# Kernel tuning notes

Hardware: AMD Instinct MI355X
Metric: run time of the kernel (lower is better)

The kernel has to match this reference:

```python
import jax, jax.numpy as jnp
import numpy as np

HID = 1024  # hidden size of the bilinear interaction space

def setup_inputs() -> dict:
    key = jax.random.key(0)
    k1, k2, kw1, kb1, kw2, kwo, kbo = jax.random.split(key, 7)
    B, N1, N2, D1, D2, OUT = 4, 128, 128, 768, 768, 2
    s1 = 1.0 / np.sqrt(D1)
    s2 = 1.0 / np.sqrt(D2)
    so = 1.0 / np.sqrt(HID)
    return {
        "input1": jax.random.normal(k1, (B, N1, D1), dtype=jnp.float32),
        "input2": jax.random.normal(k2, (B, N2, D2), dtype=jnp.float32),
        # torch nn.Linear convention: weight [out, in], y = x @ W.T + b
        "W1": jax.random.uniform(kw1, (HID, D1), jnp.float32, -s1, s1),
        "b1": jax.random.uniform(kb1, (HID,), jnp.float32, -s1, s1),
        "W2": jax.random.uniform(kw2, (HID, D2), jnp.float32, -s2, s2),  # bias=False
        "Wo": jax.random.uniform(kwo, (OUT, HID), jnp.float32, -so, so),
        "bo": jax.random.uniform(kbo, (OUT,), jnp.float32, -so, so),
    }

def reference(input1, input2, W1, b1, W2, Wo, bo):
    # in1: [B, N1, HID], in2: [B, N2, HID]
    in1 = jnp.einsum("bnd,hd->bnh", input1, W1) + b1
    in2 = jnp.einsum("bmd,hd->bmh", input2, W2)
    # broadcast outer-sum -> [B, N1, N2, HID], ReLU, then project to OUT
    h = jax.nn.relu(in1[:, :, None, :] + in2[:, None, :, :])
    return jnp.einsum("bnmh,oh->bnmo", h, Wo) + bo
```

## Files before the change

kernel.cpp:

```cpp
#include <hip/hip_runtime.h>
#include <hip/hip_bf16.h>


typedef __attribute__((ext_vector_type(8))) short s16x8;
typedef __attribute__((ext_vector_type(4))) float f32x4;

#define KP 2304
#define BK 64
#define KHALF 1152
#define NSTEP (KHALF / BK)

__device__ __forceinline__ void gl_lds16(const void* g, void* l) {
    __builtin_amdgcn_global_load_lds(
        (const __attribute__((address_space(1))) unsigned int*)g,
        (__attribute__((address_space(3))) unsigned int*)l, 16, 0, 0);
}

__global__ __launch_bounds__(256) void prepack(
    const float* __restrict__ in1, const float* __restrict__ in2,
    const float* __restrict__ W1, const float* __restrict__ W2,
    ushort* __restrict__ Abig, ushort* __restrict__ Wbig)
{
    const int gid = blockIdx.x * 256 + threadIdx.x;
    const int src = gid / 196608;
    const int rem = gid % 196608;
    const int row = rem / 192;
    const int k4  = (rem % 192) * 4;
    const float* sp;
    ushort* dst;
    if (src == 0) {
        sp  = (row < 512) ? in1 + (size_t)row * 768 + k4
                          : in2 + (size_t)(row - 512) * 768 + k4;
        dst = Abig + (size_t)row * KP + k4;
    } else {
        sp  = (src == 1 ? W1 : W2) + (size_t)row * 768 + k4;
        dst = Wbig + (size_t)(src - 1) * (1024 * KP) + (size_t)row * KP + k4;
    }
    const float4 x = *(const float4*)sp;
    const float xf[4] = {x.x, x.y, x.z, x.w};
    ushort h[4], l[4];
    #pragma unroll
    for (int i = 0; i < 4; ++i) {
        const float v = xf[i];
        __hip_bfloat16 bh = __float2bfloat16(v);
        const float fh = __bfloat162float(bh);
        __hip_bfloat16 bl = __float2bfloat16(v - fh);
        h[i] = *(ushort*)&bh;
        l[i] = *(ushort*)&bl;
    }
    const ushort4 H = make_ushort4(h[0], h[1], h[2], h[3]);
    const ushort4 L = make_ushort4(l[0], l[1], l[2], l[3]);
    if (src == 0) {
        *(ushort4*)(dst)        = H;
        *(ushort4*)(dst + 768)  = L;
        *(ushort4*)(dst + 1536) = H;
    } else {
        *(ushort4*)(dst)        = H;
        *(ushort4*)(dst + 768)  = H;
        *(ushort4*)(dst + 1536) = L;
    }
}

__global__ __launch_bounds__(512) void gemm_mfma(
    const ushort* __restrict__ Abig, const ushort* __restrict__ Wbig,
    const float* __restrict__ b1, float* __restrict__ hid)
{
    const int t    = threadIdx.x;
    const int lane = t & 63;
    const int w    = t >> 6;
    const int kh   = w >> 2;
    const int ws   = w & 3;
    const int row0 = blockIdx.y * 64;
    const int col0 = blockIdx.x * 64;

    const char* __restrict__ A = (const char*)(Abig + (size_t)row0 * KP);
    const char* __restrict__ W = (const char*)(Wbig
                                   + (row0 < 512 ? (size_t)0 : (size_t)1024 * KP)
                                   + (size_t)col0 * KP);

    __shared__ ushort lds[2][2][2][4096];

    const int srow = t >> 3;
    const int kbyt = (((t & 7) ^ (srow & 7)) << 4);
    const size_t rowoff = (size_t)srow * (KP * 2);

    const int wr = ws >> 1, wc = ws & 1;
    const int l15 = lane & 15, kg = lane >> 4;
    int aoff[2][2], boff[2][2];
    #pragma unroll
    for (int kk = 0; kk < 2; ++kk)
        #pragma unroll
        for (int f = 0; f < 2; ++f) {
            const int r = wr * 32 + f * 16 + l15;
            const int c = wc * 32 + f * 16 + l15;
            const int sw_ = kk * 64 + kg * 16;
            aoff[kk][f] = r * 128 + (sw_ ^ ((r & 7) << 4));
            boff[kk][f] = c * 128 + (sw_ ^ ((c & 7) << 4));
        }

#define STAGE(buf, ktk) do {                                                   \
        const size_t kby = (size_t)(ktk) * (BK * 2);                           \
        _Pragma("unroll")                                                      \
        for (int p = 0; p < 4; ++p) {                                          \
            const char* src = (p & 1) ? W : A;                                 \
            const size_t off = rowoff + (size_t)(p >> 1) * (KHALF * 2)         \
                               + kby + kbyt;                                   \
            gl_lds16(src + off,                                                \
                     (char*)&lds[buf][p >> 1][p & 1][0] + t * 16);             \
        }                                                                      \
    } while (0)

    const f32x4 zero = {0.f, 0.f, 0.f, 0.f};
    f32x4 acc[2][2] = {{zero, zero}, {zero, zero}};

    STAGE(0, 0);
    int cur = 0;
    for (int kt = 0; kt < NSTEP; ++kt) {
        asm volatile("s_waitcnt vmcnt(0)" ::: "memory");
        __syncthreads();
        if (kt + 1 < NSTEP) STAGE(cur ^ 1, kt + 1);
        const char* __restrict__ ab = (const char*)&lds[cur][kh][0][0];
        const char* __restrict__ wb = (const char*)&lds[cur][kh][1][0];
        #pragma unroll
        for (int kk = 0; kk < 2; ++kk) {
            s16x8 af[2], bf_[2];
            #pragma unroll
            for (int f = 0; f < 2; ++f) {
                af[f]  = *(const s16x8*)(ab + aoff[kk][f]);
                bf_[f] = *(const s16x8*)(wb + boff[kk][f]);
            }
            #pragma unroll
            for (int fr = 0; fr < 2; ++fr)
                #pragma unroll
                for (int fc = 0; fc < 2; ++fc)
                    acc[fr][fc] = __builtin_amdgcn_mfma_f32_16x16x32_bf16(
                        af[fr], bf_[fc], acc[fr][fc], 0, 0, 0);
        }
        cur ^= 1;
    }
#undef STAGE

    __syncthreads();
    float* red = (float*)&lds[0][0][0][0];
    if (kh == 1) {
        #pragma unroll
        for (int fr = 0; fr < 2; ++fr)
            #pragma unroll
            for (int fc = 0; fc < 2; ++fc)
                *(f32x4*)&red[(((ws * 2 + fr) * 2 + fc) * 64 + lane) * 4] =
                    acc[fr][fc];
    }
    __syncthreads();
    if (kh == 0) {
        float bias[2] = {0.f, 0.f};
        if (row0 < 512) {
            bias[0] = b1[col0 + wc * 32 + l15];
            bias[1] = b1[col0 + wc * 32 + 16 + l15];
        }
        #pragma unroll
        for (int fr = 0; fr < 2; ++fr)
            #pragma unroll
            for (int fc = 0; fc < 2; ++fc) {
                const f32x4 o = *(const f32x4*)
                    &red[(((ws * 2 + fr) * 2 + fc) * 64 + lane) * 4];
                #pragma unroll
                for (int i = 0; i < 4; ++i) {
                    const int r = row0 + wr * 32 + fr * 16 + kg * 4 + i;
                    const int c = col0 + wc * 32 + fc * 16 + l15;
                    hid[(size_t)r * 1024 + c] = acc[fr][fc][i] + o[i] + bias[fc];
                }
            }
    }
}

__global__ __launch_bounds__(256) void out_init(
    const float* __restrict__ bo, float* __restrict__ out)
{
    const int g = blockIdx.x * 256 + threadIdx.x;
    *(float2*)&out[(size_t)g * 2] = make_float2(bo[0], bo[1]);
}

__global__ __launch_bounds__(256) void pair_kernel(
    const float* __restrict__ hid, const float* __restrict__ Wo,
    float* __restrict__ out)
{
    const int t  = threadIdx.x;
    const int b  = blockIdx.z >> 2;
    const int h0 = (blockIdx.z & 3) * 256;
    const int n0 = blockIdx.y * 16;
    const int m0 = blockIdx.x * 16;

    __shared__ float s1[16][260];
    __shared__ float s2[16][260];
    __shared__ float sw[2][256];

    const float* __restrict__ base1 = hid + ((size_t)(b * 128 + n0)) * 1024 + h0;
    const float* __restrict__ base2 = hid + ((size_t)(512 + b * 128 + m0)) * 1024 + h0;

    #pragma unroll
    for (int p = 0; p < 4; ++p) {
        const int slot = p * 256 + t;
        const int r  = slot >> 6;
        const int c  = (slot & 63) << 2;
        *(float4*)&s1[r][c] = *(const float4*)&base1[(size_t)r * 1024 + c];
        *(float4*)&s2[r][c] = *(const float4*)&base2[(size_t)r * 1024 + c];
    }
    if (t < 128) {
        const int o = t >> 6;
        const int c = (t & 63) << 2;
        *(float4*)&sw[o][c] = *(const float4*)&Wo[(size_t)o * 1024 + h0 + c];
    }
    __syncthreads();

    const int i = t >> 4, j = t & 15;
    const float* __restrict__ xrow = &s1[i][0];
    const float* __restrict__ yrow = &s2[j][0];
    float acc0 = 0.f, acc1 = 0.f;

    #pragma unroll 8
    for (int c4 = 0; c4 < 64; ++c4) {
        const float4 x  = *(const float4*)&xrow[c4 * 4];
        const float4 y  = *(const float4*)&yrow[c4 * 4];
        const float4 uu = *(const float4*)&sw[0][c4 * 4];
        const float4 vv = *(const float4*)&sw[1][c4 * 4];
        float r;
        r = fmaxf(x.x + y.x, 0.f); acc0 = fmaf(r, uu.x, acc0); acc1 = fmaf(r, vv.x, acc1);
        r = fmaxf(x.y + y.y, 0.f); acc0 = fmaf(r, uu.y, acc0); acc1 = fmaf(r, vv.y, acc1);
        r = fmaxf(x.z + y.z, 0.f); acc0 = fmaf(r, uu.z, acc0); acc1 = fmaf(r, vv.z, acc1);
        r = fmaxf(x.w + y.w, 0.f); acc0 = fmaf(r, uu.w, acc0); acc1 = fmaf(r, vv.w, acc1);
    }

    const size_t P = (((size_t)b * 128 + n0 + i) * 128 + (m0 + j)) * 2;
    atomicAdd(&out[P],     acc0);
    atomicAdd(&out[P + 1], acc1);
}

extern "C" void kernel_launch(void* const* d_in, const int* in_sizes, int n_in,
                              void* d_out, int out_size, void* d_ws, size_t ws_size,
                              hipStream_t stream) {
    (void)in_sizes; (void)n_in; (void)out_size; (void)ws_size;
    const float* input1 = (const float*)d_in[0];
    const float* input2 = (const float*)d_in[1];
    const float* W1     = (const float*)d_in[2];
    const float* b1     = (const float*)d_in[3];
    const float* W2     = (const float*)d_in[4];
    const float* Wo     = (const float*)d_in[5];
    const float* bo     = (const float*)d_in[6];
    float* out = (float*)d_out;

    ushort* Abig = (ushort*)d_ws;
    ushort* Wbig = Abig + (size_t)1024 * KP;
    float*  hid  = (float*)(Wbig + (size_t)2 * 1024 * KP);

    prepack<<<2304, 256, 0, stream>>>(input1, input2, W1, W2, Abig, Wbig);
    gemm_mfma<<<dim3(16, 16), 512, 0, stream>>>(Abig, Wbig, b1, hid);
    out_init<<<256, 256, 0, stream>>>(bo, out);
    pair_kernel<<<dim3(8, 8, 16), 256, 0, stream>>>(hid, Wo, out);
}
```

Baseline: 105.9 us.

## Split GEMM K dimension across blocks with atomic accumulation into bias-initialized output

Replaces the in-block two-way K split (512 threads, LDS reduction) with a 6-way split-K across the grid's z dimension, so the GEMM launches 1536 blocks of 256 threads instead of 256 blocks. A new init kernel pre-fills the hidden buffer with the bias (or zero for the second input), and each block atomically adds its partial tile. The double-buffered async prefetch is dropped in favor of a single-buffer load-sync-compute loop. This is meant to fill more compute units, at the cost of an extra kernel launch, float atomics traffic, nondeterministic summation order, and no load/compute overlap inside a block.

```diff
diff --git a/kernel.cpp b/kernel.cpp
--- a/kernel.cpp
+++ b/kernel.cpp
@@ -7,13 +7,25 @@
 
 #define KP 2304
 #define BK 64
-#define KHALF 1152
-#define NSTEP (KHALF / BK)
+#define KSPLIT 6
+#define KRANGE 384
+#define NSTEPK (KRANGE / BK)
 
 __device__ __forceinline__ void gl_lds16(const void* g, void* l) {
     __builtin_amdgcn_global_load_lds(
         (const __attribute__((address_space(1))) unsigned int*)g,
         (__attribute__((address_space(3))) unsigned int*)l, 16, 0, 0);
+}
+
+__global__ __launch_bounds__(256) void hid_init(
+    const float* __restrict__ b1, float* __restrict__ hid)
+{
+    const int g   = blockIdx.x * 256 + threadIdx.x;
+    const int row = g >> 8;
+    const int c4  = (g & 255) << 2;
+    float4 v = make_float4(0.f, 0.f, 0.f, 0.f);
+    if (row < 512) v = *(const float4*)&b1[c4];
+    *(float4*)&hid[(size_t)row * 1024 + c4] = v;
 }
 
 __global__ __launch_bounds__(256) void prepack(
@@ -61,30 +73,33 @@
     }
 }
 
-__global__ __launch_bounds__(512) void gemm_mfma(
+__global__ __launch_bounds__(256) void gemm_mfma(
     const ushort* __restrict__ Abig, const ushort* __restrict__ Wbig,
-    const float* __restrict__ b1, float* __restrict__ hid)
+    float* __restrict__ hid)
 {
     const int t    = threadIdx.x;
     const int lane = t & 63;
     const int w    = t >> 6;
-    const int kh   = w >> 2;
-    const int ws   = w & 3;
     const int row0 = blockIdx.y * 64;
     const int col0 = blockIdx.x * 64;
-
-    const char* __restrict__ A = (const char*)(Abig + (size_t)row0 * KP);
+    const int k0   = blockIdx.z * KRANGE;
+
+    const char* __restrict__ A = (const char*)(Abig + (size_t)row0 * KP + k0);
     const char* __restrict__ W = (const char*)(Wbig
                                    + (row0 < 512 ? (size_t)0 : (size_t)1024 * KP)
-                                   + (size_t)col0 * KP);
-
-    __shared__ ushort lds[2][2][2][4096];
-
-    const int srow = t >> 3;
-    const int kbyt = (((t & 7) ^ (srow & 7)) << 4);
-    const size_t rowoff = (size_t)srow * (KP * 2);
-
-    const int wr = ws >> 1, wc = ws & 1;
+                                   + (size_t)col0 * KP + k0);
+
+    __shared__ ushort lds[2][4096];
+
+    int srow[2], cbyt[2];
+    #pragma unroll
+    for (int q = 0; q < 2; ++q) {
+        const int slot = q * 256 + t;
+        srow[q] = slot >> 3;
+        cbyt[q] = ((slot & 7) ^ (srow[q] & 7)) << 4;
+    }
+
+    const int wr = w >> 1, wc = w & 1;
     const int l15 = lane & 15, kg = lane >> 4;
     int aoff[2][2], boff[2][2];
     #pragma unroll
@@ -98,36 +113,25 @@
             boff[kk][f] = c * 128 + (sw_ ^ ((c & 7) << 4));
         }
 
-#define STAGE(buf, ktk) do {                                                   \
-        const size_t kby = (size_t)(ktk) * (BK * 2);                           \
-        _Pragma("unroll")                                                      \
-        for (int p = 0; p < 4; ++p) {                                          \
-            const char* src = (p & 1) ? W : A;                                 \
-            const size_t off = rowoff + (size_t)(p >> 1) * (KHALF * 2)         \
-                               + kby + kbyt;                                   \
-            gl_lds16(src + off,                                                \
-                     (char*)&lds[buf][p >> 1][p & 1][0] + t * 16);             \
-        }                                                                      \
-    } while (0)
-
     const f32x4 zero = {0.f, 0.f, 0.f, 0.f};
     f32x4 acc[2][2] = {{zero, zero}, {zero, zero}};
 
-    STAGE(0, 0);
-    int cur = 0;
-    for (int kt = 0; kt < NSTEP; ++kt) {
-        asm volatile("s_waitcnt vmcnt(0)" ::: "memory");
+    for (int kt = 0; kt < NSTEPK; ++kt) {
+        #pragma unroll
+        for (int q = 0; q < 2; ++q) {
+            const size_t off = (size_t)srow[q] * (KP * 2) + kt * (BK * 2) + cbyt[q];
+            const int dst = (q * 256 + t) * 16;
+            gl_lds16(A + off, (char*)&lds[0][0] + dst);
+            gl_lds16(W + off, (char*)&lds[1][0] + dst);
+        }
         __syncthreads();
-        if (kt + 1 < NSTEP) STAGE(cur ^ 1, kt + 1);
-        const char* __restrict__ ab = (const char*)&lds[cur][kh][0][0];
-        const char* __restrict__ wb = (const char*)&lds[cur][kh][1][0];
         #pragma unroll
         for (int kk = 0; kk < 2; ++kk) {
             s16x8 af[2], bf_[2];
             #pragma unroll
             for (int f = 0; f < 2; ++f) {
-                af[f]  = *(const s16x8*)(ab + aoff[kk][f]);
-                bf_[f] = *(const s16x8*)(wb + boff[kk][f]);
+                af[f]  = *(const s16x8*)((const char*)&lds[0][0] + aoff[kk][f]);
+                bf_[f] = *(const s16x8*)((const char*)&lds[1][0] + boff[kk][f]);
             }
             #pragma unroll
             for (int fr = 0; fr < 2; ++fr)
@@ -136,41 +140,19 @@
                     acc[fr][fc] = __builtin_amdgcn_mfma_f32_16x16x32_bf16(
                         af[fr], bf_[fc], acc[fr][fc], 0, 0, 0);
         }
-        cur ^= 1;
-    }
-#undef STAGE
-
-    __syncthreads();
-    float* red = (float*)&lds[0][0][0][0];
-    if (kh == 1) {
-        #pragma unroll
-        for (int fr = 0; fr < 2; ++fr)
+        __syncthreads();
+    }
+
+    #pragma unroll
+    for (int fr = 0; fr < 2; ++fr)
+        #pragma unroll
+        for (int fc = 0; fc < 2; ++fc)
             #pragma unroll
-            for (int fc = 0; fc < 2; ++fc)
-                *(f32x4*)&red[(((ws * 2 + fr) * 2 + fc) * 64 + lane) * 4] =
-                    acc[fr][fc];
-    }
-    __syncthreads();
-    if (kh == 0) {
-        float bias[2] = {0.f, 0.f};
-        if (row0 < 512) {
-            bias[0] = b1[col0 + wc * 32 + l15];
-            bias[1] = b1[col0 + wc * 32 + 16 + l15];
-        }
-        #pragma unroll
-        for (int fr = 0; fr < 2; ++fr)
-            #pragma unroll
-            for (int fc = 0; fc < 2; ++fc) {
-                const f32x4 o = *(const f32x4*)
-                    &red[(((ws * 2 + fr) * 2 + fc) * 64 + lane) * 4];
-                #pragma unroll
-                for (int i = 0; i < 4; ++i) {
-                    const int r = row0 + wr * 32 + fr * 16 + kg * 4 + i;
-                    const int c = col0 + wc * 32 + fc * 16 + l15;
-                    hid[(size_t)r * 1024 + c] = acc[fr][fc][i] + o[i] + bias[fc];
-                }
+            for (int i = 0; i < 4; ++i) {
+                const int r = row0 + wr * 32 + fr * 16 + kg * 4 + i;
+                const int c = col0 + wc * 32 + fc * 16 + l15;
+                atomicAdd(&hid[(size_t)r * 1024 + c], acc[fr][fc][i]);
             }
-    }
 }
 
 __global__ __launch_bounds__(256) void out_init(
@@ -252,8 +234,9 @@
     ushort* Wbig = Abig + (size_t)1024 * KP;
     float*  hid  = (float*)(Wbig + (size_t)2 * 1024 * KP);
 
+    hid_init<<<1024, 256, 0, stream>>>(b1, hid);
     prepack<<<2304, 256, 0, stream>>>(input1, input2, W1, W2, Abig, Wbig);
-    gemm_mfma<<<dim3(16, 16), 512, 0, stream>>>(Abig, Wbig, b1, hid);
+    gemm_mfma<<<dim3(16, 16, KSPLIT), 256, 0, stream>>>(Abig, Wbig, hid);
     out_init<<<256, 256, 0, stream>>>(bo, out);
     pair_kernel<<<dim3(8, 8, 16), 256, 0, stream>>>(hid, Wo, out);
 }
```

Result: slower. 116.3 us (+9.9%).
